# Performance work log

Measured on AMD Instinct MI355X. Metric: run time of the kernel, lower is better.

Reference implementation:

```python
import jax, jax.numpy as jnp
import numpy as np

N_NODES = 100000
N_EDGES = 1600000


def sgconv(x, src, dst, W, b, K=1):
    """PyG SGConv: K hops of GCN-normalized propagation, then Linear."""
    n = x.shape[0]
    # add self loops
    loop = jnp.arange(n, dtype=src.dtype)
    s = jnp.concatenate([src, loop])  # source (j)
    d = jnp.concatenate([dst, loop])  # target (i)
    # symmetric normalization: deg over targets of A+I
    deg = jax.ops.segment_sum(jnp.ones_like(d, dtype=x.dtype), d, num_segments=n)
    dinv = jnp.where(deg > 0, jax.lax.rsqrt(deg), 0.0)
    norm = dinv[s] * dinv[d]  # [E+N]
    for _ in range(K):
        msg = x[s] * norm[:, None]  # gather + scale  [E+N, F]
        x = jax.ops.segment_sum(msg, d, num_segments=n)  # scatter-add
    return x @ W + b


def setup_inputs() -> dict:
    key = jax.random.key(0)
    k1, k2, k3, k4, k5, k6, k7 = jax.random.split(key, 7)
    x = jax.random.normal(k1, (N_NODES, 128), dtype=jnp.float32)
    edge_index = jax.random.randint(k2, (2, N_EDGES), 0, N_NODES, dtype=jnp.int64)
    # Glorot-ish scaled weights
    W1 = jax.random.normal(k3, (128, 128), dtype=jnp.float32) * (1.0 / np.sqrt(128))
    b1 = jax.random.normal(k4, (128,), dtype=jnp.float32) * 0.01
    W2 = jax.random.normal(k5, (128, 64), dtype=jnp.float32) * (1.0 / np.sqrt(128))
    b2 = jax.random.normal(k6, (64,), dtype=jnp.float32) * 0.01
    return {"x": x, "edge_index": edge_index, "W1": W1, "b1": b1, "W2": W2, "b2": b2}


def reference(x, edge_index, W1, b1, W2, b2):
    src, dst = edge_index[0], edge_index[1]
    h = sgconv(x, src, dst, W1, b1, K=1)
    out = sgconv(h, src, dst, W2, b2, K=1)
    return out
```

## Files before the change

kernel.cpp:

```cpp
#include <hip/hip_runtime.h>

#define NN 100000
#define NE 1600000
#define BSH 9
#define NPB (1 << BSH)
#define NBKT ((NN + NPB - 1) >> BSH)
#define ABLK 400
#define EPB (NE / ABLK)
#define CAP 10240

typedef __attribute__((ext_vector_type(8))) short short8;
typedef __attribute__((ext_vector_type(4))) float f32x4;

__device__ __forceinline__ unsigned short bf16r(float f) {
    unsigned u = __float_as_uint(f);
    u += 0x7fffu + ((u >> 16) & 1u);
    return (unsigned short)(u >> 16);
}
__device__ __forceinline__ unsigned pack2(float a, float b) {
    unsigned ua = __float_as_uint(a), ub = __float_as_uint(b);
    ua += 0x7fffu + ((ua >> 16) & 1u);
    ub += 0x7fffu + ((ub >> 16) & 1u);
    return (ua >> 16) | (ub & 0xffff0000u);
}
__device__ __forceinline__ float2 unpack2(unsigned u) {
    float2 r;
    r.x = __uint_as_float(u << 16);
    r.y = __uint_as_float(u & 0xffff0000u);
    return r;
}

__global__ __launch_bounds__(256) void k_scat2(const int* __restrict__ src,
                                               const int* __restrict__ dst,
                                               unsigned* __restrict__ cur,
                                               unsigned* __restrict__ epk) {
    __shared__ unsigned hcnt[NBKT];
    __shared__ unsigned hbase[NBKT];
    int b = blockIdx.x, t = threadIdx.x;
    for (int k = t; k < NBKT; k += 256) hcnt[k] = 0;
    __syncthreads();
    int e0 = b * EPB;
    for (int e = e0 + t; e < e0 + EPB; e += 256)
        atomicAdd(&hcnt[(unsigned)dst[e] >> BSH], 1u);
    __syncthreads();
    for (int k = t; k < NBKT; k += 256) {
        unsigned c = hcnt[k];
        hbase[k] = k * CAP + (c ? atomicAdd(&cur[k], c) : 0u);
        hcnt[k] = 0;
    }
    __syncthreads();
    for (int e = e0 + t; e < e0 + EPB; e += 256) {
        unsigned d = (unsigned)dst[e];
        unsigned kb = d >> BSH;
        unsigned pos = hbase[kb] + atomicAdd(&hcnt[kb], 1u);
        epk[pos] = ((d & (NPB - 1)) << 17) | (unsigned)src[e];
    }
}

__global__ __launch_bounds__(512) void k_csrB2(const unsigned* __restrict__ cur,
                                               const unsigned* __restrict__ epk,
                                               int* __restrict__ csr, int* __restrict__ off,
                                               int* __restrict__ deg, float* __restrict__ dinv,
                                               const float* __restrict__ W1,
                                               const float* __restrict__ W2,
                                               const float* __restrict__ b1,
                                               unsigned short* __restrict__ W12b,
                                               float* __restrict__ c2) {
    int blk = blockIdx.x;
    if (blk >= NBKT) {
        int idx = (blk - NBKT) * 512 + threadIdx.x;
        if (idx < 8192) {
            int i = idx >> 6, j = idx & 63;
            float acc = 0.f;
            for (int k = 0; k < 128; ++k) acc += W1[i * 128 + k] * W2[k * 64 + j];
            W12b[j * 128 + i] = bf16r(acc);
        } else if (idx < 8192 + 64) {
            int j = idx - 8192;
            float acc = 0.f;
            for (int k = 0; k < 128; ++k) acc += b1[k] * W2[k * 64 + j];
            c2[j] = acc;
        }
        return;
    }
    __shared__ unsigned lcnt[NPB];
    __shared__ unsigned lcur[NPB];
    __shared__ unsigned wtot[8];
    int k = blk, t = threadIdx.x;
    int lane = t & 63, wv = t >> 6;
    unsigned e0 = (unsigned)k * CAP, e1 = e0 + cur[k];
    lcnt[t] = 0;
    __syncthreads();
    for (unsigned e = e0 + t; e < e1; e += NPB)
        atomicAdd(&lcnt[epk[e] >> 17], 1u);
    __syncthreads();
    unsigned own = lcnt[t];
    unsigned sum = own;
    #pragma unroll
    for (int d = 1; d < 64; d <<= 1) {
        unsigned v = __shfl_up(sum, d, 64);
        if (lane >= d) sum += v;
    }
    if (lane == 63) wtot[wv] = sum;
    __syncthreads();
    if (t == 0) {
        unsigned acc = 0;
        #pragma unroll
        for (int i = 0; i < 8; ++i) { unsigned v = wtot[i]; wtot[i] = acc; acc += v; }
    }
    __syncthreads();
    unsigned excl = wtot[wv] + sum - own;
    int n = k * NPB + t;
    if (n < NN) {
        off[n]  = (int)(e0 + excl);
        deg[n]  = (int)own;
        dinv[n] = rsqrtf((float)own + 1.0f);
    }
    lcur[t] = excl;
    __syncthreads();
    for (unsigned e = e0 + t; e < e1; e += NPB) {
        unsigned u = epk[e];
        unsigned pos = atomicAdd(&lcur[u >> 17], 1u);
        csr[e0 + pos] = (int)(u & 0x1FFFFu);
    }
}

__global__ __launch_bounds__(256) void k_gemmYs(const float* __restrict__ x,
                                                const unsigned short* __restrict__ W12b,
                                                const float* __restrict__ dinv,
                                                unsigned short* __restrict__ ys) {
    __shared__ float Al[64][132];
    __shared__ short Wl[64][136];
    int t = threadIdx.x;
    int row0 = blockIdx.x * 64;

    for (int idx8 = t; idx8 < 1024; idx8 += 256) {
        int n = idx8 >> 4, c8 = idx8 & 15;
        *(short8*)&Wl[n][c8 * 8] = *(const short8*)&W12b[n * 128 + c8 * 8];
    }
    for (int idx = t; idx < 64 * 32; idx += 256) {
        int r = idx >> 5, c4 = idx & 31;
        float4 v = make_float4(0.f, 0.f, 0.f, 0.f);
        if (row0 + r < NN) v = *(const float4*)&x[(size_t)(row0 + r) * 128 + c4 * 4];
        *(float4*)&Al[r][c4 * 4] = v;
    }
    __syncthreads();

    int wv = t >> 6, lane = t & 63;
    int l15 = lane & 15, l4 = lane >> 4;

    short8 afr[4];
    #pragma unroll
    for (int ks = 0; ks < 4; ++ks) {
        const float* ap = &Al[wv * 16 + l15][ks * 32 + l4 * 8];
        float4 f0 = *(const float4*)ap;
        float4 f1 = *(const float4*)(ap + 4);
        short8 a;
        a[0] = (short)bf16r(f0.x); a[1] = (short)bf16r(f0.y);
        a[2] = (short)bf16r(f0.z); a[3] = (short)bf16r(f0.w);
        a[4] = (short)bf16r(f1.x); a[5] = (short)bf16r(f1.y);
        a[6] = (short)bf16r(f1.z); a[7] = (short)bf16r(f1.w);
        afr[ks] = a;
    }
    short8 bfr[4][4];
    #pragma unroll
    for (int ct = 0; ct < 4; ++ct)
        #pragma unroll
        for (int ks = 0; ks < 4; ++ks)
            bfr[ct][ks] = *(const short8*)&Wl[ct * 16 + l15][ks * 32 + l4 * 8];

    f32x4 acc[4] = {};
    #pragma unroll
    for (int ks = 0; ks < 4; ++ks)
        #pragma unroll
        for (int ct = 0; ct < 4; ++ct)
            acc[ct] = __builtin_amdgcn_mfma_f32_16x16x32_bf16(afr[ks], bfr[ct][ks], acc[ct], 0, 0, 0);

    int rbase = row0 + wv * 16 + l4 * 4;
    float di[4];
    #pragma unroll
    for (int r = 0; r < 4; ++r) di[r] = (rbase + r < NN) ? dinv[rbase + r] : 0.f;
    #pragma unroll
    for (int ct = 0; ct < 4; ++ct) {
        int col = ct * 16 + l15;
        #pragma unroll
        for (int r = 0; r < 4; ++r) {
            if (rbase + r < NN)
                ys[(size_t)(rbase + r) * 64 + col] = bf16r(acc[ct][r] * di[r]);
        }
    }
}

__global__ __launch_bounds__(256) void k_gatherA(const int* __restrict__ off,
        const int* __restrict__ deg, const int* __restrict__ csr,
        const float* __restrict__ dinv, const uint4* __restrict__ ys4,
        const float* __restrict__ c2, uint4* __restrict__ ts4) {
    int gid = blockIdx.x * blockDim.x + threadIdx.x;
    int node = gid >> 3;
    int lane = threadIdx.x & 7;
    if (node >= NN) return;
    uint4 u = ys4[(size_t)node * 8 + lane];
    float2 p0 = unpack2(u.x), p1 = unpack2(u.y), p2 = unpack2(u.z), p3 = unpack2(u.w);
    float a0 = p0.x, a1 = p0.y, a2 = p1.x, a3 = p1.y;
    float a4 = p2.x, a5 = p2.y, a6 = p3.x, a7 = p3.y;
    int e = off[node], end = e + deg[node];
    for (; e + 8 <= end; e += 8) {
        uint4 v[8];
        #pragma unroll
        for (int j = 0; j < 8; ++j) v[j] = ys4[(size_t)csr[e + j] * 8 + lane];
        #pragma unroll
        for (int j = 0; j < 8; ++j) {
            float2 t0 = unpack2(v[j].x), t1 = unpack2(v[j].y);
            float2 t2 = unpack2(v[j].z), t3 = unpack2(v[j].w);
            a0 += t0.x; a1 += t0.y; a2 += t1.x; a3 += t1.y;
            a4 += t2.x; a5 += t2.y; a6 += t3.x; a7 += t3.y;
        }
    }
    for (; e + 4 <= end; e += 4) {
        uint4 v[4];
        #pragma unroll
        for (int j = 0; j < 4; ++j) v[j] = ys4[(size_t)csr[e + j] * 8 + lane];
        #pragma unroll
        for (int j = 0; j < 4; ++j) {
            float2 t0 = unpack2(v[j].x), t1 = unpack2(v[j].y);
            float2 t2 = unpack2(v[j].z), t3 = unpack2(v[j].w);
            a0 += t0.x; a1 += t0.y; a2 += t1.x; a3 += t1.y;
            a4 += t2.x; a5 += t2.y; a6 += t3.x; a7 += t3.y;
        }
    }
    for (; e < end; ++e) {
        uint4 v = ys4[(size_t)csr[e] * 8 + lane];
        float2 t0 = unpack2(v.x), t1 = unpack2(v.y);
        float2 t2 = unpack2(v.z), t3 = unpack2(v.w);
        a0 += t0.x; a1 += t0.y; a2 += t1.x; a3 += t1.y;
        a4 += t2.x; a5 += t2.y; a6 += t3.x; a7 += t3.y;
    }
    float di = dinv[node];
    float s = di * di;
    float4 cA = ((const float4*)c2)[lane * 2];
    float4 cB = ((const float4*)c2)[lane * 2 + 1];
    ts4[(size_t)node * 8 + lane] = make_uint4(
        pack2(s * a0 + di * cA.x, s * a1 + di * cA.y),
        pack2(s * a2 + di * cA.z, s * a3 + di * cA.w),
        pack2(s * a4 + di * cB.x, s * a5 + di * cB.y),
        pack2(s * a6 + di * cB.z, s * a7 + di * cB.w));
}

__global__ __launch_bounds__(256) void k_gatherB(const int* __restrict__ off,
        const int* __restrict__ deg, const int* __restrict__ csr,
        const float* __restrict__ dinv, const uint4* __restrict__ ts4,
        const float* __restrict__ bias, float* __restrict__ out) {
    int gid = blockIdx.x * blockDim.x + threadIdx.x;
    int node = gid >> 3;
    int lane = threadIdx.x & 7;
    if (node >= NN) return;
    uint4 u = ts4[(size_t)node * 8 + lane];
    float2 p0 = unpack2(u.x), p1 = unpack2(u.y), p2 = unpack2(u.z), p3 = unpack2(u.w);
    float a0 = p0.x, a1 = p0.y, a2 = p1.x, a3 = p1.y;
    float a4 = p2.x, a5 = p2.y, a6 = p3.x, a7 = p3.y;
    int e = off[node], end = e + deg[node];
    for (; e + 8 <= end; e += 8) {
        uint4 v[8];
        #pragma unroll
        for (int j = 0; j < 8; ++j) v[j] = ts4[(size_t)csr[e + j] * 8 + lane];
        #pragma unroll
        for (int j = 0; j < 8; ++j) {
            float2 t0 = unpack2(v[j].x), t1 = unpack2(v[j].y);
            float2 t2 = unpack2(v[j].z), t3 = unpack2(v[j].w);
            a0 += t0.x; a1 += t0.y; a2 += t1.x; a3 += t1.y;
            a4 += t2.x; a5 += t2.y; a6 += t3.x; a7 += t3.y;
        }
    }
    for (; e + 4 <= end; e += 4) {
        uint4 v[4];
        #pragma unroll
        for (int j = 0; j < 4; ++j) v[j] = ts4[(size_t)csr[e + j] * 8 + lane];
        #pragma unroll
        for (int j = 0; j < 4; ++j) {
            float2 t0 = unpack2(v[j].x), t1 = unpack2(v[j].y);
            float2 t2 = unpack2(v[j].z), t3 = unpack2(v[j].w);
            a0 += t0.x; a1 += t0.y; a2 += t1.x; a3 += t1.y;
            a4 += t2.x; a5 += t2.y; a6 += t3.x; a7 += t3.y;
        }
    }
    for (; e < end; ++e) {
        uint4 v = ts4[(size_t)csr[e] * 8 + lane];
        float2 t0 = unpack2(v.x), t1 = unpack2(v.y);
        float2 t2 = unpack2(v.z), t3 = unpack2(v.w);
        a0 += t0.x; a1 += t0.y; a2 += t1.x; a3 += t1.y;
        a4 += t2.x; a5 += t2.y; a6 += t3.x; a7 += t3.y;
    }
    float di = dinv[node];
    float4 bA = ((const float4*)bias)[lane * 2];
    float4 bB = ((const float4*)bias)[lane * 2 + 1];
    float* op = out + (size_t)node * 64 + lane * 8;
    *(float4*)op       = make_float4(a0 * di + bA.x, a1 * di + bA.y,
                                     a2 * di + bA.z, a3 * di + bA.w);
    *(float4*)(op + 4) = make_float4(a4 * di + bB.x, a5 * di + bB.y,
                                     a6 * di + bB.z, a7 * di + bB.w);
}

extern "C" void kernel_launch(void* const* d_in, const int* in_sizes, int n_in,
                              void* d_out, int out_size, void* d_ws, size_t ws_size,
                              hipStream_t stream) {
    const float* x  = (const float*)d_in[0];
    const int*   ei = (const int*)d_in[1];
    const float* W1 = (const float*)d_in[2];
    const float* b1 = (const float*)d_in[3];
    const float* W2 = (const float*)d_in[4];
    const float* b2 = (const float*)d_in[5];
    float* out = (float*)d_out;

    const int* src = ei;
    const int* dst = ei + NE;

    float* fws  = (float*)d_ws;
    float* dinv = fws;
    unsigned* ys = (unsigned*)(fws + 102400);
    unsigned* ts = ys + (size_t)NN * 32;
    unsigned short* W12b = (unsigned short*)(ts + (size_t)NN * 32);
    float* c2   = (float*)(W12b + 8192);
    int* off  = (int*)(c2 + 128);
    int* deg  = off + 100096;
    int* csr  = deg + 100096;
    unsigned* epk = (unsigned*)(csr + NBKT * CAP);
    unsigned* cur = epk + NBKT * CAP;

    hipMemsetAsync(cur, 0, NBKT * sizeof(unsigned), stream);
    k_scat2<<<ABLK, 256, 0, stream>>>(src, dst, cur, epk);
    k_csrB2<<<NBKT + 17, 512, 0, stream>>>(cur, epk, csr, off, deg, dinv,
                                           W1, W2, b1, W12b, c2);

    k_gemmYs<<<(NN + 63) / 64, 256, 0, stream>>>(x, W12b, dinv, (unsigned short*)ys);

    k_gatherA<<<(NN * 8 + 255) / 256, 256, 0, stream>>>(off, deg, csr, dinv,
                                                        (const uint4*)ys, c2, (uint4*)ts);

    k_gatherB<<<(NN * 8 + 255) / 256, 256, 0, stream>>>(off, deg, csr, dinv,
                                                        (const uint4*)ts, b2, out);
}
```

Before: 136.9 us.

## Stage bucketed edges in shared memory before coalesced global write-out

The edge bucketing kernel now computes a block-local prefix sum of bucket counts, places packed edges into a shared-memory buffer sorted by bucket, and then writes them to global memory in contiguous runs, using a binary search over bucket offsets to find each element's bucket. This aims to replace scattered per-edge global stores with mostly contiguous writes per bucket. The cost is a 16KB shared buffer per block, extra synchronizations and a binary search per element. It assumes NBKT is at most 256, which holds for 196 buckets.

```diff
diff --git a/kernel.cpp b/kernel.cpp
--- a/kernel.cpp
+++ b/kernel.cpp
@@ -30,30 +30,62 @@
     return r;
 }
 
-__global__ __launch_bounds__(256) void k_scat2(const int* __restrict__ src,
+__global__ __launch_bounds__(256) void k_scat3(const int* __restrict__ src,
                                                const int* __restrict__ dst,
                                                unsigned* __restrict__ cur,
                                                unsigned* __restrict__ epk) {
-    __shared__ unsigned hcnt[NBKT];
-    __shared__ unsigned hbase[NBKT];
-    int b = blockIdx.x, t = threadIdx.x;
-    for (int k = t; k < NBKT; k += 256) hcnt[k] = 0;
-    __syncthreads();
-    int e0 = b * EPB;
+    __shared__ unsigned hcnt[256];
+    __shared__ unsigned hloc[256];
+    __shared__ unsigned gbase[256];
+    __shared__ unsigned wtot[4];
+    __shared__ unsigned ebuf[EPB];
+    const int b = blockIdx.x, t = threadIdx.x;
+    const int lane = t & 63, wv = t >> 6;
+    const int e0 = b * EPB;
+
+    hcnt[t] = 0;
+    __syncthreads();
+    #pragma unroll 1
     for (int e = e0 + t; e < e0 + EPB; e += 256)
         atomicAdd(&hcnt[(unsigned)dst[e] >> BSH], 1u);
     __syncthreads();
-    for (int k = t; k < NBKT; k += 256) {
-        unsigned c = hcnt[k];
-        hbase[k] = k * CAP + (c ? atomicAdd(&cur[k], c) : 0u);
-        hcnt[k] = 0;
-    }
-    __syncthreads();
+    unsigned own = hcnt[t];
+    unsigned sum = own;
+    #pragma unroll
+    for (int d = 1; d < 64; d <<= 1) {
+        unsigned v = __shfl_up(sum, d, 64);
+        if (lane >= d) sum += v;
+    }
+    if (lane == 63) wtot[wv] = sum;
+    __syncthreads();
+    if (t == 0) {
+        unsigned acc = 0;
+        #pragma unroll
+        for (int i = 0; i < 4; ++i) { unsigned v = wtot[i]; wtot[i] = acc; acc += v; }
+    }
+    __syncthreads();
+    unsigned excl = wtot[wv] + sum - own;
+    hloc[t] = excl;
+    if (t < NBKT)
+        gbase[t] = t * CAP + (own ? atomicAdd(&cur[t], own) : 0u);
+    hcnt[t] = excl;
+    __syncthreads();
+    #pragma unroll 1
     for (int e = e0 + t; e < e0 + EPB; e += 256) {
         unsigned d = (unsigned)dst[e];
-        unsigned kb = d >> BSH;
-        unsigned pos = hbase[kb] + atomicAdd(&hcnt[kb], 1u);
-        epk[pos] = ((d & (NPB - 1)) << 17) | (unsigned)src[e];
+        unsigned pos = atomicAdd(&hcnt[d >> BSH], 1u);
+        ebuf[pos] = ((d & (NPB - 1)) << 17) | (unsigned)src[e];
+    }
+    __syncthreads();
+    #pragma unroll 1
+    for (int i = t; i < EPB; i += 256) {
+        int k = 0;
+        #pragma unroll
+        for (int step = 128; step; step >>= 1) {
+            int cand = k + step;
+            if (cand < 256 && hloc[cand] <= (unsigned)i) k = cand;
+        }
+        epk[gbase[k] + (i - hloc[k])] = ebuf[i];
     }
 }
 
@@ -326,7 +358,7 @@
     unsigned* cur = epk + NBKT * CAP;
 
     hipMemsetAsync(cur, 0, NBKT * sizeof(unsigned), stream);
-    k_scat2<<<ABLK, 256, 0, stream>>>(src, dst, cur, epk);
+    k_scat3<<<ABLK, 256, 0, stream>>>(src, dst, cur, epk);
     k_csrB2<<<NBKT + 17, 512, 0, stream>>>(cur, epk, csr, off, deg, dinv,
                                            W1, W2, b1, W12b, c2);
 
```

Result: slower. 139.6 us (+2.0%).

## Sort nodes by degree within buckets to balance gather wavefront work

Applied to the files above, without the earlier changes.

Builds a per-bucket permutation of node ids sorted by in-degree, using a shared-memory degree histogram and prefix scan in the CSR build kernel. Both gather kernels then process nodes in that order, so the nodes sharing a wavefront have similar edge counts. This is meant to reduce divergence and idle lanes caused by uneven degrees. It adds an order array write and read plus padding positions that exit early, and output writes become scattered within each bucket.

```diff
diff --git a/kernel.cpp b/kernel.cpp
--- a/kernel.cpp
+++ b/kernel.cpp
@@ -8,6 +8,7 @@
 #define ABLK 400
 #define EPB (NE / ABLK)
 #define CAP 10240
+#define NPOS (NBKT * NPB)
 
 typedef __attribute__((ext_vector_type(8))) short short8;
 typedef __attribute__((ext_vector_type(4))) float f32x4;
@@ -61,6 +62,7 @@
                                                const unsigned* __restrict__ epk,
                                                int* __restrict__ csr, int* __restrict__ off,
                                                int* __restrict__ deg, float* __restrict__ dinv,
+                                               int* __restrict__ order,
                                                const float* __restrict__ W1,
                                                const float* __restrict__ W2,
                                                const float* __restrict__ b1,
@@ -85,10 +87,13 @@
     __shared__ unsigned lcnt[NPB];
     __shared__ unsigned lcur[NPB];
     __shared__ unsigned wtot[8];
+    __shared__ unsigned dh[64];
     int k = blk, t = threadIdx.x;
     int lane = t & 63, wv = t >> 6;
     unsigned e0 = (unsigned)k * CAP, e1 = e0 + cur[k];
     lcnt[t] = 0;
+    if (t < 64) dh[t] = 0;
+    order[k * NPB + t] = 0x7FFFFFFF;
     __syncthreads();
     for (unsigned e = e0 + t; e < e1; e += NPB)
         atomicAdd(&lcnt[epk[e] >> 17], 1u);
@@ -110,13 +115,29 @@
     __syncthreads();
     unsigned excl = wtot[wv] + sum - own;
     int n = k * NPB + t;
+    unsigned dcl = own < 63u ? own : 63u;
     if (n < NN) {
         off[n]  = (int)(e0 + excl);
         deg[n]  = (int)own;
         dinv[n] = rsqrtf((float)own + 1.0f);
+        atomicAdd(&dh[dcl], 1u);
     }
     lcur[t] = excl;
     __syncthreads();
+    if (t < 64) {
+        unsigned v = dh[t], s2 = v;
+        #pragma unroll
+        for (int d = 1; d < 64; d <<= 1) {
+            unsigned u = __shfl_up(s2, d, 64);
+            if (t >= d) s2 += u;
+        }
+        dh[t] = s2 - v;
+    }
+    __syncthreads();
+    if (n < NN) {
+        unsigned r = atomicAdd(&dh[dcl], 1u);
+        order[k * NPB + r] = n;
+    }
     for (unsigned e = e0 + t; e < e1; e += NPB) {
         unsigned u = epk[e];
         unsigned pos = atomicAdd(&lcur[u >> 17], 1u);
@@ -190,13 +211,16 @@
     }
 }
 
-__global__ __launch_bounds__(256) void k_gatherA(const int* __restrict__ off,
-        const int* __restrict__ deg, const int* __restrict__ csr,
-        const float* __restrict__ dinv, const uint4* __restrict__ ys4,
-        const float* __restrict__ c2, uint4* __restrict__ ts4) {
+__global__ __launch_bounds__(256) void k_gatherA(const int* __restrict__ order,
+        const int* __restrict__ off, const int* __restrict__ deg,
+        const int* __restrict__ csr, const float* __restrict__ dinv,
+        const uint4* __restrict__ ys4, const float* __restrict__ c2,
+        uint4* __restrict__ ts4) {
     int gid = blockIdx.x * blockDim.x + threadIdx.x;
-    int node = gid >> 3;
+    int pos = gid >> 3;
     int lane = threadIdx.x & 7;
+    if (pos >= NPOS) return;
+    int node = order[pos];
     if (node >= NN) return;
     uint4 u = ys4[(size_t)node * 8 + lane];
     float2 p0 = unpack2(u.x), p1 = unpack2(u.y), p2 = unpack2(u.z), p3 = unpack2(u.w);
@@ -245,13 +269,16 @@
         pack2(s * a6 + di * cB.z, s * a7 + di * cB.w));
 }
 
-__global__ __launch_bounds__(256) void k_gatherB(const int* __restrict__ off,
-        const int* __restrict__ deg, const int* __restrict__ csr,
-        const float* __restrict__ dinv, const uint4* __restrict__ ts4,
-        const float* __restrict__ bias, float* __restrict__ out) {
+__global__ __launch_bounds__(256) void k_gatherB(const int* __restrict__ order,
+        const int* __restrict__ off, const int* __restrict__ deg,
+        const int* __restrict__ csr, const float* __restrict__ dinv,
+        const uint4* __restrict__ ts4, const float* __restrict__ bias,
+        float* __restrict__ out) {
     int gid = blockIdx.x * blockDim.x + threadIdx.x;
-    int node = gid >> 3;
+    int pos = gid >> 3;
     int lane = threadIdx.x & 7;
+    if (pos >= NPOS) return;
+    int node = order[pos];
     if (node >= NN) return;
     uint4 u = ts4[(size_t)node * 8 + lane];
     float2 p0 = unpack2(u.x), p1 = unpack2(u.y), p2 = unpack2(u.z), p3 = unpack2(u.w);
@@ -324,17 +351,18 @@
     int* csr  = deg + 100096;
     unsigned* epk = (unsigned*)(csr + NBKT * CAP);
     unsigned* cur = epk + NBKT * CAP;
+    int* order = (int*)(cur + 256);
 
     hipMemsetAsync(cur, 0, NBKT * sizeof(unsigned), stream);
     k_scat2<<<ABLK, 256, 0, stream>>>(src, dst, cur, epk);
-    k_csrB2<<<NBKT + 17, 512, 0, stream>>>(cur, epk, csr, off, deg, dinv,
+    k_csrB2<<<NBKT + 17, 512, 0, stream>>>(cur, epk, csr, off, deg, dinv, order,
                                            W1, W2, b1, W12b, c2);
 
     k_gemmYs<<<(NN + 63) / 64, 256, 0, stream>>>(x, W12b, dinv, (unsigned short*)ys);
 
-    k_gatherA<<<(NN * 8 + 255) / 256, 256, 0, stream>>>(off, deg, csr, dinv,
-                                                        (const uint4*)ys, c2, (uint4*)ts);
-
-    k_gatherB<<<(NN * 8 + 255) / 256, 256, 0, stream>>>(off, deg, csr, dinv,
-                                                        (const uint4*)ts, b2, out);
-}
+    k_gatherA<<<(NPOS * 8 + 255) / 256, 256, 0, stream>>>(order, off, deg, csr, dinv,
+                                                          (const uint4*)ys, c2, (uint4*)ts);
+
+    k_gatherB<<<(NPOS * 8 + 255) / 256, 256, 0, stream>>>(order, off, deg, csr, dinv,
+                                                          (const uint4*)ts, b2, out);
+}
```

After: 151.1 us. +10.4%, slower.
